# Kernel optimization log

Measured on AMD Instinct MI355X. Metric: run time of the kernel, lower is better.

## Reference

```python
import jax, jax.numpy as jnp
import numpy as np

B, S, D = 2, 2048, 2048
NQ, NKV = 16, 4
HD = D // NQ           # 128
GROUP = NQ // NKV      # 4


def setup_inputs() -> dict:
    key = jax.random.key(0)
    k_x, k_q, k_k, k_v, k_o = jax.random.split(key, 5)
    scale = 0.02
    return {
        "x": jax.random.normal(k_x, (B, S, D), dtype=jnp.float32),
        # torch nn.Linear weights have shape (out_features, in_features)
        "Wq": jax.random.normal(k_q, (D, D), dtype=jnp.float32) * scale,
        "Wk": jax.random.normal(k_k, (NKV * HD, D), dtype=jnp.float32) * scale,
        "Wv": jax.random.normal(k_v, (NKV * HD, D), dtype=jnp.float32) * scale,
        "Wo": jax.random.normal(k_o, (D, D), dtype=jnp.float32) * scale,
    }


def reference(x, Wq, Wk, Wv, Wo):
    b, s, _ = x.shape
    # projections (Linear: x @ W.T), then split heads -> (b, h, s, hd)
    Q = (x @ Wq.T).reshape(b, s, NQ, HD).transpose(0, 2, 1, 3)
    K = (x @ Wk.T).reshape(b, s, NKV, HD).transpose(0, 2, 1, 3)
    V = (x @ Wv.T).reshape(b, s, NKV, HD).transpose(0, 2, 1, 3)
    # GQA: broadcast each KV head across its query-head group (repeat_interleave on head dim)
    K = jnp.repeat(K, GROUP, axis=1)  # (b, NQ, s, hd)
    V = jnp.repeat(V, GROUP, axis=1)
    scores = jnp.einsum("bhqd,bhkd->bhqk", Q, K) / jnp.sqrt(jnp.float32(HD))
    causal = jnp.triu(jnp.ones((s, s), dtype=bool), k=1)  # True above diagonal -> masked
    scores = jnp.where(causal, -jnp.inf, scores)
    weights = jax.nn.softmax(scores, axis=-1)  # dropout p=0.0 -> identity
    ctx = jnp.einsum("bhqk,bhkd->bhqd", weights, V)
    ctx = ctx.transpose(0, 2, 1, 3).reshape(b, s, D)
    return ctx @ Wo.T
```

## Files before the change

### kernel.cpp

```cpp
#include <hip/hip_runtime.h>
#include <stdint.h>

#define S_LEN 2048
#define DMODEL 2048
#define NQH 16
#define NKVH 4
#define HDK 128

typedef __bf16 bf16x8 __attribute__((ext_vector_type(8)));
typedef float f32x4 __attribute__((ext_vector_type(4)));
typedef float f32x16 __attribute__((ext_vector_type(16)));

__device__ __forceinline__ void async16(const void* g, void* l) {
  __builtin_amdgcn_global_load_lds((const __attribute__((address_space(1))) void*)g,
                                   (__attribute__((address_space(3))) void*)l,
                                   16, 0, 0);
}

__device__ __forceinline__ f32x4 mfma16(bf16x8 a, bf16x8 b, f32x4 c) {
  return __builtin_amdgcn_mfma_f32_16x16x32_bf16(a, b, c, 0, 0, 0);
}
__device__ __forceinline__ f32x16 mfma32(bf16x8 a, bf16x8 b, f32x16 c) {
  return __builtin_amdgcn_mfma_f32_32x32x16_bf16(a, b, c, 0, 0, 0);
}
__device__ __forceinline__ uint32_t pkbf16(float lo, float hi) {
  uint32_t r;
  asm("v_cvt_pk_bf16_f32 %0, %1, %2" : "=v"(r) : "v"(lo), "v"(hi));
  return r;
}

__global__ __launch_bounds__(256) void cvt_all(
    const float* __restrict__ i0, const float* __restrict__ i1,
    const float* __restrict__ i2, const float* __restrict__ i3,
    const float* __restrict__ i4, __bf16* __restrict__ o0,
    __bf16* __restrict__ o1, __bf16* __restrict__ o2, __bf16* __restrict__ o3,
    __bf16* __restrict__ o4) {
  int v = blockIdx.x * 256 + threadIdx.x;
  const float* in;
  __bf16* out;
  int base;
  if (v < 1048576)      { in = i0; out = o0; base = 0; }
  else if (v < 1572864) { in = i1; out = o1; base = 1048576; }
  else if (v < 1703936) { in = i2; out = o2; base = 1572864; }
  else if (v < 1835008) { in = i3; out = o3; base = 1703936; }
  else                  { in = i4; out = o4; base = 1835008; }
  int i = (v - base) * 8;
  const float4* p = (const float4*)(in + i);
  float4 a = p[0], b = p[1];
  bf16x8 o;
  o[0] = (__bf16)a.x; o[1] = (__bf16)a.y; o[2] = (__bf16)a.z; o[3] = (__bf16)a.w;
  o[4] = (__bf16)b.x; o[5] = (__bf16)b.y; o[6] = (__bf16)b.z; o[7] = (__bf16)b.w;
  *(bf16x8*)(out + i) = o;
}

template <bool F32OUT>
__global__ __launch_bounds__(256) void gemm_bt(const __bf16* __restrict__ A,
                                               const __bf16* __restrict__ B0,
                                               const __bf16* __restrict__ B1,
                                               const __bf16* __restrict__ B2,
                                               void* __restrict__ C0,
                                               void* __restrict__ C1,
                                               void* __restrict__ C2,
                                               int Ntot, int Ns1, int Ns2, int K) {
  int nbn = Ntot >> 7;
  int nwg = gridDim.x;
  int bid = blockIdx.x;
  int bx = (bid & 7) * (nwg >> 3) + (bid >> 3);
  int m0 = (bx / nbn) << 7;
  int n0g = (bx % nbn) << 7;
  const __bf16* B;
  void* C;
  int n0, Nc;
  if (n0g < Ns1)      { B = B0; C = C0; n0 = n0g;       Nc = Ns1; }
  else if (n0g < Ns2) { B = B1; C = C1; n0 = n0g - Ns1; Nc = Ns2 - Ns1; }
  else                { B = B2; C = C2; n0 = n0g - Ns2; Nc = Ntot - Ns2; }

  __shared__ __align__(16) uint8_t As[16384];
  __shared__ __align__(16) uint8_t Bs[16384];

  int t = threadIdx.x, lane = t & 63, w = t >> 6;
  int wr = w >> 1, wc = w & 1;
  f32x4 acc[4][4] = {};

  for (int k0 = 0; k0 < K; k0 += 64) {
#pragma unroll
    for (int i = 0; i < 4; ++i) {
      int c = (i << 8) + t;
      int row = c >> 3;
      int colb = ((c & 7) << 4) ^ ((row & 7) << 4);
      async16((const uint8_t*)(A + (size_t)(m0 + row) * K + k0) + colb, As + c * 16);
      async16((const uint8_t*)(B + (size_t)(n0 + row) * K + k0) + colb, Bs + c * 16);
    }
    __syncthreads();
#pragma unroll
    for (int ks = 0; ks < 2; ++ks) {
      bf16x8 af[4], bfr[4];
#pragma unroll
      for (int m = 0; m < 4; ++m) {
        int row = wr * 64 + m * 16 + (lane & 15);
        int colb = ((ks << 6) + ((lane >> 4) << 4)) ^ ((row & 7) << 4);
        af[m] = *(const bf16x8*)(As + row * 128 + colb);
      }
#pragma unroll
      for (int n = 0; n < 4; ++n) {
        int row = wc * 64 + n * 16 + (lane & 15);
        int colb = ((ks << 6) + ((lane >> 4) << 4)) ^ ((row & 7) << 4);
        bfr[n] = *(const bf16x8*)(Bs + row * 128 + colb);
      }
      __builtin_amdgcn_s_setprio(1);
#pragma unroll
      for (int m = 0; m < 4; ++m)
#pragma unroll
        for (int n = 0; n < 4; ++n)
          acc[m][n] = mfma16(af[m], bfr[n], acc[m][n]);
      __builtin_amdgcn_s_setprio(0);
    }
    __syncthreads();
  }
#pragma unroll
  for (int m = 0; m < 4; ++m)
#pragma unroll
    for (int n = 0; n < 4; ++n)
#pragma unroll
      for (int j = 0; j < 4; ++j) {
        int mg = m0 + wr * 64 + m * 16 + ((lane >> 4) << 2) + j;
        int ng = n0 + wc * 64 + n * 16 + (lane & 15);
        float v = acc[m][n][j];
        if (F32OUT) ((float*)C)[(size_t)mg * Nc + ng] = v;
        else        ((__bf16*)C)[(size_t)mg * Nc + ng] = (__bf16)v;
      }
}

__global__ __launch_bounds__(256) void transpose_v(const __bf16* __restrict__ V,
                                                   __bf16* __restrict__ Vt) {
  int bid = blockIdx.x;
  int dt = bid & 1, st = (bid >> 1) & 31, kvh = (bid >> 6) & 3, b = bid >> 8;
  __shared__ __align__(16) __bf16 tile[64][72];
  int t = threadIdx.x;
#pragma unroll
  for (int i = 0; i < 2; ++i) {
    int c = (i << 8) + t;
    int sr = c >> 3, cb = (c & 7) << 3;
    bf16x8 v = *(const bf16x8*)(V + (size_t)(b * S_LEN + st * 64 + sr) * 512 +
                                kvh * HDK + dt * 64 + cb);
    *(bf16x8*)(&tile[sr][cb]) = v;
  }
  __syncthreads();
#pragma unroll
  for (int i = 0; i < 2; ++i) {
    int c = (i << 8) + t;
    int dr = c >> 3, sb = (c & 7) << 3;
    bf16x8 o;
#pragma unroll
    for (int j = 0; j < 8; ++j) o[j] = tile[sb + j][dr];
    *(bf16x8*)(Vt + (size_t)((b * NKVH + kvh) * HDK + dt * 64 + dr) * S_LEN +
               st * 64 + sb) = o;
  }
}

__global__ __launch_bounds__(256, 2) void attn(const __bf16* __restrict__ Q,
                                               const __bf16* __restrict__ Kx,
                                               const __bf16* __restrict__ Vt,
                                               __bf16* __restrict__ Ctx) {
  int bid0 = blockIdx.x;
  int bid = ((bid0 & 7) << 6) | (bid0 >> 3);
  int qt = 15 - (bid & 15);
  int h = (bid >> 4) & 15;
  int b = bid >> 8;
  int kvh = h >> 2;
  int q0 = qt << 7;
  int t = threadIdx.x, lane = t & 63, w = t >> 6;
  int qr = lane & 31;
  int hi = lane >> 5;
  int qwb = q0 + (w << 5);

  __shared__ __align__(16) uint8_t Ks[2][16384];
  __shared__ __align__(16) uint8_t Vs[2][16384];

  const __bf16* kbase = Kx + (size_t)b * S_LEN * 512 + kvh * HDK;
  const __bf16* vbase = Vt + (size_t)(b * NKVH + kvh) * HDK * S_LEN;

  auto stage = [&](int kt, int bufi) {
#pragma unroll
    for (int i = 0; i < 4; ++i) {
      int c = (i << 8) + t;
      int krow = c >> 4;
      int kcolb = ((c & 15) << 4) ^ ((krow & 7) << 4);
      async16((const uint8_t*)(kbase + (size_t)((kt << 6) + krow) * 512) + kcolb,
              Ks[bufi] + c * 16);
      int vrow = c >> 3;
      int vcolb = ((c & 7) << 4) ^ ((vrow & 7) << 4);
      async16((const uint8_t*)(vbase + (size_t)vrow * S_LEN + (kt << 6)) + vcolb,
              Vs[bufi] + c * 16);
    }
  };

  int NT = (qt << 1) + 2;
  stage(0, 0);

  bf16x8 qf[8];
  {
    const __bf16* qrow = Q + (size_t)(b * S_LEN + qwb + qr) * DMODEL + h * HDK + hi * 8;
#pragma unroll
    for (int dk = 0; dk < 8; ++dk) qf[dk] = *(const bf16x8*)(qrow + dk * 16);
  }
  __syncthreads();

  const float NEG = -3.0e38f;
  const float SC = 0.08838834764831845f;
  float m_run = NEG, l_run = 0.f;
  f32x16 acc[4] = {};

  for (int kt = 0; kt < NT; ++kt) {
    int cur = kt & 1;
    if (kt + 1 < NT) stage(kt + 1, cur ^ 1);
    int k0 = kt << 6;
    if (k0 <= qwb + 31) {
      const uint8_t* ks = Ks[cur];
      const uint8_t* vs = Vs[cur];

      f32x16 st0 = {}, st1 = {};
      __builtin_amdgcn_s_setprio(1);
#pragma unroll
      for (int dk = 0; dk < 8; ++dk) {
        int cb = (dk << 5) + (hi << 4);
        int swz = (qr & 7) << 4;
        bf16x8 kf0 = *(const bf16x8*)(ks + qr * 256 + (cb ^ swz));
        st0 = mfma32(kf0, qf[dk], st0);
        bf16x8 kf1 = *(const bf16x8*)(ks + (32 + qr) * 256 + (cb ^ swz));
        st1 = mfma32(kf1, qf[dk], st1);
      }
      __builtin_amdgcn_s_setprio(0);

      if (k0 + 63 > qwb) {
#pragma unroll
        for (int r = 0; r < 16; ++r) {
          int kl = (r & 3) + ((r >> 2) << 3) + (hi << 2);
          st0[r] = (k0 + kl > qwb + qr) ? NEG : st0[r];
          st1[r] = (k0 + 32 + kl > qwb + qr) ? NEG : st1[r];
        }
      }

      float tm[16];
#pragma unroll
      for (int r = 0; r < 16; ++r) tm[r] = fmaxf(st0[r], st1[r]);
#pragma unroll
      for (int s = 8; s > 0; s >>= 1)
#pragma unroll
        for (int r = 0; r < s; ++r) tm[r] = fmaxf(tm[r], tm[r + s]);
      float mx = fmaxf(tm[0], __shfl_xor(tm[0], 32, 64));

      if (__any(mx > m_run + 90.52f)) {
        float mn = fmaxf(m_run, mx);
        float al = __expf((m_run - mn) * SC);
        l_run *= al;
        m_run = mn;
#pragma unroll
        for (int i = 0; i < 16; ++i) {
          float alr = __shfl(al, (i & 3) + ((i >> 2) << 3) + (hi << 2), 64);
          acc[0][i] *= alr; acc[1][i] *= alr; acc[2][i] *= alr; acc[3][i] *= alr;
        }
      }

      float mSC = m_run * SC;
      float p0[16], p1[16];
#pragma unroll
      for (int r = 0; r < 16; ++r) p0[r] = __expf(fmaf(st0[r], SC, -mSC));
#pragma unroll
      for (int r = 0; r < 16; ++r) p1[r] = __expf(fmaf(st1[r], SC, -mSC));
      float ts[16];
#pragma unroll
      for (int r = 0; r < 16; ++r) ts[r] = p0[r] + p1[r];
#pragma unroll
      for (int s = 8; s > 0; s >>= 1)
#pragma unroll
        for (int r = 0; r < s; ++r) ts[r] += ts[r + s];
      l_run += ts[0] + __shfl_xor(ts[0], 32, 64);

      uint32_t wd0[4][2], wd1[4][2];
#pragma unroll
      for (int g = 0; g < 4; ++g) {
        wd0[g][0] = pkbf16(p0[4 * g + 0], p0[4 * g + 1]);
        wd0[g][1] = pkbf16(p0[4 * g + 2], p0[4 * g + 3]);
        wd1[g][0] = pkbf16(p1[4 * g + 0], p1[4 * g + 1]);
        wd1[g][1] = pkbf16(p1[4 * g + 2], p1[4 * g + 3]);
      }
      bf16x8 pa[4];
#define PEXCH(WD, IDX0, IDX1)                                                  \
      {                                                                        \
        uint32_t s0 = hi ? WD[0][0] : WD[1][0];                                \
        uint32_t s1 = hi ? WD[0][1] : WD[1][1];                                \
        uint32_t s2 = hi ? WD[2][0] : WD[3][0];                                \
        uint32_t s3 = hi ? WD[2][1] : WD[3][1];                                \
        uint32_t r0 = (uint32_t)__shfl_xor((int)s0, 32, 64);                   \
        uint32_t r1 = (uint32_t)__shfl_xor((int)s1, 32, 64);                   \
        uint32_t r2 = (uint32_t)__shfl_xor((int)s2, 32, 64);                   \
        uint32_t r3 = (uint32_t)__shfl_xor((int)s3, 32, 64);                   \
        union { bf16x8 v; uint32_t u[4]; } fa, fb;                             \
        fa.u[0] = hi ? r0 : WD[0][0];                                          \
        fa.u[1] = hi ? r1 : WD[0][1];                                          \
        fa.u[2] = hi ? WD[1][0] : r0;                                          \
        fa.u[3] = hi ? WD[1][1] : r1;                                          \
        fb.u[0] = hi ? r2 : WD[2][0];                                          \
        fb.u[1] = hi ? r3 : WD[2][1];                                          \
        fb.u[2] = hi ? WD[3][0] : r2;                                          \
        fb.u[3] = hi ? WD[3][1] : r3;                                          \
        pa[IDX0] = fa.v;                                                       \
        pa[IDX1] = fb.v;                                                       \
      }
      PEXCH(wd0, 0, 1)
      PEXCH(wd1, 2, 3)
#undef PEXCH

      __builtin_amdgcn_s_setprio(1);
#pragma unroll
      for (int dt = 0; dt < 4; ++dt) {
        int row = (dt << 5) + qr;
        int swz = (row & 7) << 4;
#pragma unroll
        for (int kc = 0; kc < 4; ++kc) {
          bf16x8 vf = *(const bf16x8*)(vs + row * 128 + (((kc << 5) + (hi << 4)) ^ swz));
          acc[dt] = mfma32(pa[kc], vf, acc[dt]);
        }
      }
      __builtin_amdgcn_s_setprio(0);
    }
    __syncthreads();
  }

#pragma unroll
  for (int i = 0; i < 16; ++i) {
    int rm = (i & 3) + ((i >> 2) << 3) + (hi << 2);
    float lr = __shfl(l_run, rm, 64);
    float inv = 1.0f / lr;
    size_t rowoff = (size_t)(b * S_LEN + qwb + rm) * DMODEL + h * HDK + qr;
#pragma unroll
    for (int dt = 0; dt < 4; ++dt)
      Ctx[rowoff + (dt << 5)] = (__bf16)(acc[dt][i] * inv);
  }
}

extern "C" void kernel_launch(void* const* d_in, const int* in_sizes, int n_in,
                              void* d_out, int out_size, void* d_ws, size_t ws_size,
                              hipStream_t stream) {
  const float* x  = (const float*)d_in[0];
  const float* Wq = (const float*)d_in[1];
  const float* Wk = (const float*)d_in[2];
  const float* Wv = (const float*)d_in[3];
  const float* Wo = (const float*)d_in[4];
  float* out = (float*)d_out;

  const size_t MB = 1024 * 1024;
  uint8_t* ws = (uint8_t*)d_ws;
  __bf16* xb  = (__bf16*)(ws + 0 * MB);
  __bf16* Wqb = (__bf16*)(ws + 16 * MB);
  __bf16* Wkb = (__bf16*)(ws + 24 * MB);
  __bf16* Wvb = (__bf16*)(ws + 26 * MB);
  __bf16* Wob = (__bf16*)(ws + 28 * MB);
  __bf16* Qb  = (__bf16*)(ws + 36 * MB);
  __bf16* Kb  = (__bf16*)(ws + 52 * MB);
  __bf16* Vb  = (__bf16*)(ws + 56 * MB);
  __bf16* Vtb = (__bf16*)(ws + 60 * MB);
  __bf16* Ctx = (__bf16*)(ws + 64 * MB);

  cvt_all<<<9216, 256, 0, stream>>>(x, Wq, Wk, Wv, Wo, xb, Wqb, Wkb, Wvb, Wob);

  gemm_bt<false><<<(4096 / 128) * (3072 / 128), 256, 0, stream>>>(
      xb, Wqb, Wkb, Wvb, (void*)Qb, (void*)Kb, (void*)Vb, 3072, 2048, 2560, 2048);

  transpose_v<<<512, 256, 0, stream>>>(Vb, Vtb);

  attn<<<2 * 16 * 16, 256, 0, stream>>>(Qb, Kb, Vtb, Ctx);

  gemm_bt<true><<<(4096 / 128) * (2048 / 128), 256, 0, stream>>>(
      Ctx, Wob, Wob, Wob, (void*)out, (void*)out, (void*)out, 2048, 2048, 2048, 2048);
}
```

Before: 200.1 us.

## Split attention KV tile across two wave groups with shared-memory softmax merge

The attention block grows to 512 threads. The two halves of the block each process one 32-key half of every 64-key tile for the same 128 query rows. At the end, the halves merge their running max, running sum and accumulators through LDS, reusing the K/V staging buffers. This doubles the waves working on each query tile to improve latency hiding and per-CU occupancy. It costs an extra merge step, more LDS traffic, and 4 blocks per CU under the launch bounds, which may force register spills.

```diff
diff --git a/kernel.cpp b/kernel.cpp
--- a/kernel.cpp
+++ b/kernel.cpp
@@ -158,7 +158,7 @@
   }
 }
 
-__global__ __launch_bounds__(256, 2) void attn(const __bf16* __restrict__ Q,
+__global__ __launch_bounds__(512, 4) void attn(const __bf16* __restrict__ Q,
                                                const __bf16* __restrict__ Kx,
                                                const __bf16* __restrict__ Vt,
                                                __bf16* __restrict__ Ctx) {
@@ -170,20 +170,23 @@
   int kvh = h >> 2;
   int q0 = qt << 7;
   int t = threadIdx.x, lane = t & 63, w = t >> 6;
+  int half = w >> 2, wq = w & 3;
   int qr = lane & 31;
   int hi = lane >> 5;
-  int qwb = q0 + (w << 5);
+  int qwb = q0 + (wq << 5);
+  int kofs = half << 5;
 
   __shared__ __align__(16) uint8_t Ks[2][16384];
   __shared__ __align__(16) uint8_t Vs[2][16384];
+  __shared__ float MLs[4][2][32];
 
   const __bf16* kbase = Kx + (size_t)b * S_LEN * 512 + kvh * HDK;
   const __bf16* vbase = Vt + (size_t)(b * NKVH + kvh) * HDK * S_LEN;
 
   auto stage = [&](int kt, int bufi) {
 #pragma unroll
-    for (int i = 0; i < 4; ++i) {
-      int c = (i << 8) + t;
+    for (int i = 0; i < 2; ++i) {
+      int c = (i << 9) + t;
       int krow = c >> 4;
       int kcolb = ((c & 15) << 4) ^ ((krow & 7) << 4);
       async16((const uint8_t*)(kbase + (size_t)((kt << 6) + krow) * 512) + kcolb,
@@ -215,37 +218,34 @@
     int cur = kt & 1;
     if (kt + 1 < NT) stage(kt + 1, cur ^ 1);
     int k0 = kt << 6;
-    if (k0 <= qwb + 31) {
+    if (k0 + kofs <= qwb + 31) {
       const uint8_t* ks = Ks[cur];
       const uint8_t* vs = Vs[cur];
 
-      f32x16 st0 = {}, st1 = {};
+      f32x16 st = {};
+      int swz = (qr & 7) << 4;
       __builtin_amdgcn_s_setprio(1);
 #pragma unroll
       for (int dk = 0; dk < 8; ++dk) {
-        int cb = (dk << 5) + (hi << 4);
-        int swz = (qr & 7) << 4;
-        bf16x8 kf0 = *(const bf16x8*)(ks + qr * 256 + (cb ^ swz));
-        st0 = mfma32(kf0, qf[dk], st0);
-        bf16x8 kf1 = *(const bf16x8*)(ks + (32 + qr) * 256 + (cb ^ swz));
-        st1 = mfma32(kf1, qf[dk], st1);
+        bf16x8 kf = *(const bf16x8*)(ks + (kofs + qr) * 256 +
+                                     (((dk << 5) + (hi << 4)) ^ swz));
+        st = mfma32(kf, qf[dk], st);
       }
       __builtin_amdgcn_s_setprio(0);
 
-      if (k0 + 63 > qwb) {
+      if (k0 + kofs + 31 > qwb) {
 #pragma unroll
         for (int r = 0; r < 16; ++r) {
           int kl = (r & 3) + ((r >> 2) << 3) + (hi << 2);
-          st0[r] = (k0 + kl > qwb + qr) ? NEG : st0[r];
-          st1[r] = (k0 + 32 + kl > qwb + qr) ? NEG : st1[r];
+          st[r] = (k0 + kofs + kl > qwb + qr) ? NEG : st[r];
         }
       }
 
-      float tm[16];
-#pragma unroll
-      for (int r = 0; r < 16; ++r) tm[r] = fmaxf(st0[r], st1[r]);
-#pragma unroll
-      for (int s = 8; s > 0; s >>= 1)
+      float tm[8];
+#pragma unroll
+      for (int r = 0; r < 8; ++r) tm[r] = fmaxf(st[r], st[r + 8]);
+#pragma unroll
+      for (int s = 4; s > 0; s >>= 1)
 #pragma unroll
         for (int r = 0; r < s; ++r) tm[r] = fmaxf(tm[r], tm[r + s]);
       float mx = fmaxf(tm[0], __shfl_xor(tm[0], 32, 64));
@@ -263,63 +263,56 @@
       }
 
       float mSC = m_run * SC;
-      float p0[16], p1[16];
-#pragma unroll
-      for (int r = 0; r < 16; ++r) p0[r] = __expf(fmaf(st0[r], SC, -mSC));
-#pragma unroll
-      for (int r = 0; r < 16; ++r) p1[r] = __expf(fmaf(st1[r], SC, -mSC));
-      float ts[16];
-#pragma unroll
-      for (int r = 0; r < 16; ++r) ts[r] = p0[r] + p1[r];
-#pragma unroll
-      for (int s = 8; s > 0; s >>= 1)
+      float p0[16];
+#pragma unroll
+      for (int r = 0; r < 16; ++r) p0[r] = __expf(fmaf(st[r], SC, -mSC));
+      float ts[8];
+#pragma unroll
+      for (int r = 0; r < 8; ++r) ts[r] = p0[r] + p0[r + 8];
+#pragma unroll
+      for (int s = 4; s > 0; s >>= 1)
 #pragma unroll
         for (int r = 0; r < s; ++r) ts[r] += ts[r + s];
       l_run += ts[0] + __shfl_xor(ts[0], 32, 64);
 
-      uint32_t wd0[4][2], wd1[4][2];
+      uint32_t wd0[4][2];
 #pragma unroll
       for (int g = 0; g < 4; ++g) {
         wd0[g][0] = pkbf16(p0[4 * g + 0], p0[4 * g + 1]);
         wd0[g][1] = pkbf16(p0[4 * g + 2], p0[4 * g + 3]);
-        wd1[g][0] = pkbf16(p1[4 * g + 0], p1[4 * g + 1]);
-        wd1[g][1] = pkbf16(p1[4 * g + 2], p1[4 * g + 3]);
-      }
-      bf16x8 pa[4];
-#define PEXCH(WD, IDX0, IDX1)                                                  \
-      {                                                                        \
-        uint32_t s0 = hi ? WD[0][0] : WD[1][0];                                \
-        uint32_t s1 = hi ? WD[0][1] : WD[1][1];                                \
-        uint32_t s2 = hi ? WD[2][0] : WD[3][0];                                \
-        uint32_t s3 = hi ? WD[2][1] : WD[3][1];                                \
-        uint32_t r0 = (uint32_t)__shfl_xor((int)s0, 32, 64);                   \
-        uint32_t r1 = (uint32_t)__shfl_xor((int)s1, 32, 64);                   \
-        uint32_t r2 = (uint32_t)__shfl_xor((int)s2, 32, 64);                   \
-        uint32_t r3 = (uint32_t)__shfl_xor((int)s3, 32, 64);                   \
-        union { bf16x8 v; uint32_t u[4]; } fa, fb;                             \
-        fa.u[0] = hi ? r0 : WD[0][0];                                          \
-        fa.u[1] = hi ? r1 : WD[0][1];                                          \
-        fa.u[2] = hi ? WD[1][0] : r0;                                          \
-        fa.u[3] = hi ? WD[1][1] : r1;                                          \
-        fb.u[0] = hi ? r2 : WD[2][0];                                          \
-        fb.u[1] = hi ? r3 : WD[2][1];                                          \
-        fb.u[2] = hi ? WD[3][0] : r2;                                          \
-        fb.u[3] = hi ? WD[3][1] : r3;                                          \
-        pa[IDX0] = fa.v;                                                       \
-        pa[IDX1] = fb.v;                                                       \
-      }
-      PEXCH(wd0, 0, 1)
-      PEXCH(wd1, 2, 3)
-#undef PEXCH
+      }
+      bf16x8 pa[2];
+      {
+        uint32_t s0 = hi ? wd0[0][0] : wd0[1][0];
+        uint32_t s1 = hi ? wd0[0][1] : wd0[1][1];
+        uint32_t s2 = hi ? wd0[2][0] : wd0[3][0];
+        uint32_t s3 = hi ? wd0[2][1] : wd0[3][1];
+        uint32_t r0 = (uint32_t)__shfl_xor((int)s0, 32, 64);
+        uint32_t r1 = (uint32_t)__shfl_xor((int)s1, 32, 64);
+        uint32_t r2 = (uint32_t)__shfl_xor((int)s2, 32, 64);
+        uint32_t r3 = (uint32_t)__shfl_xor((int)s3, 32, 64);
+        union { bf16x8 v; uint32_t u[4]; } fa, fb;
+        fa.u[0] = hi ? r0 : wd0[0][0];
+        fa.u[1] = hi ? r1 : wd0[0][1];
+        fa.u[2] = hi ? wd0[1][0] : r0;
+        fa.u[3] = hi ? wd0[1][1] : r1;
+        fb.u[0] = hi ? r2 : wd0[2][0];
+        fb.u[1] = hi ? r3 : wd0[2][1];
+        fb.u[2] = hi ? wd0[3][0] : r2;
+        fb.u[3] = hi ? wd0[3][1] : r3;
+        pa[0] = fa.v;
+        pa[1] = fb.v;
+      }
 
       __builtin_amdgcn_s_setprio(1);
 #pragma unroll
       for (int dt = 0; dt < 4; ++dt) {
         int row = (dt << 5) + qr;
-        int swz = (row & 7) << 4;
-#pragma unroll
-        for (int kc = 0; kc < 4; ++kc) {
-          bf16x8 vf = *(const bf16x8*)(vs + row * 128 + (((kc << 5) + (hi << 4)) ^ swz));
+        int swzv = (row & 7) << 4;
+#pragma unroll
+        for (int kc = 0; kc < 2; ++kc) {
+          bf16x8 vf = *(const bf16x8*)(
+              vs + row * 128 + (((kofs << 1) + (kc << 5) + (hi << 4)) ^ swzv));
           acc[dt] = mfma32(pa[kc], vf, acc[dt]);
         }
       }
@@ -328,15 +321,40 @@
     __syncthreads();
   }
 
-#pragma unroll
-  for (int i = 0; i < 16; ++i) {
-    int rm = (i & 3) + ((i >> 2) << 3) + (hi << 2);
-    float lr = __shfl(l_run, rm, 64);
-    float inv = 1.0f / lr;
-    size_t rowoff = (size_t)(b * S_LEN + qwb + rm) * DMODEL + h * HDK + qr;
+  float* obuf = (wq < 2) ? (float*)(&Ks[0][0] + wq * 16384)
+                         : (float*)(&Vs[0][0] + (wq - 2) * 16384);
+  if (half) {
+    if (hi == 0) { MLs[wq][0][qr] = m_run; MLs[wq][1][qr] = l_run; }
 #pragma unroll
     for (int dt = 0; dt < 4; ++dt)
-      Ctx[rowoff + (dt << 5)] = (__bf16)(acc[dt][i] * inv);
+#pragma unroll
+      for (int i4 = 0; i4 < 4; ++i4) {
+        f32x4 v4 = {acc[dt][i4 * 4 + 0], acc[dt][i4 * 4 + 1],
+                    acc[dt][i4 * 4 + 2], acc[dt][i4 * 4 + 3]};
+        *(f32x4*)(obuf + dt * 1024 + lane * 16 + i4 * 4) = v4;
+      }
+  }
+  __syncthreads();
+  if (!half) {
+    float m1 = MLs[wq][0][qr], l1 = MLs[wq][1][qr];
+    float ms = fmaxf(m_run, m1);
+    float a0 = __expf((m_run - ms) * SC);
+    float a1 = __expf((m1 - ms) * SC);
+    float linv = 1.f / (l_run * a0 + l1 * a1);
+#pragma unroll
+    for (int i = 0; i < 16; ++i) {
+      int rm = (i & 3) + ((i >> 2) << 3) + (hi << 2);
+      float a0r = __shfl(a0, rm, 64);
+      float a1r = __shfl(a1, rm, 64);
+      float invr = __shfl(linv, rm, 64);
+      size_t rowoff = (size_t)(b * S_LEN + qwb + rm) * DMODEL + h * HDK + qr;
+#pragma unroll
+      for (int dt = 0; dt < 4; ++dt) {
+        float o1 = obuf[dt * 1024 + lane * 16 + i];
+        Ctx[rowoff + (dt << 5)] =
+            (__bf16)((acc[dt][i] * a0r + o1 * a1r) * invr);
+      }
+    }
   }
 }
 
@@ -370,7 +388,7 @@
 
   transpose_v<<<512, 256, 0, stream>>>(Vb, Vtb);
 
-  attn<<<2 * 16 * 16, 256, 0, stream>>>(Qb, Kb, Vtb, Ctx);
+  attn<<<512, 512, 0, stream>>>(Qb, Kb, Vtb, Ctx);
 
   gemm_bt<true><<<(4096 / 128) * (2048 / 128), 256, 0, stream>>>(
       Ctx, Wob, Wob, Wob, (void*)out, (void*)out, (void*)out, 2048, 2048, 2048, 2048);
```

Result: slower. 275.2 us (+37.6%).
